# Kernel tuning notes

Measured on AMD Instinct MI355X. Metric: run time of the kernel, lower is better.

Reference implementation:

```python
import jax, jax.numpy as jnp
from jax import lax
import numpy as np

D = 1024   # hidden_size
N = 8      # num_experts
K = 2      # num_chosen_experts
KS = 1     # num_shared_experts
H = 2 * D  # hidden_ratio * D
B, S = 2, 1024


def setup_inputs() -> dict:
    key = jax.random.key(0)
    k1, k2, k3, k4 = jax.random.split(key, 4)
    scale = 1.0 / np.sqrt(D).astype(np.float32)
    x = jax.random.normal(k1, (B, S, D), dtype=jnp.float32)
    Wg = jax.random.normal(k2, (D, N), dtype=jnp.float32) * scale
    Wl1 = jax.random.normal(k3, (N, D, 2 * H), dtype=jnp.float32) * scale
    Wl2 = jax.random.normal(k4, (N, H, D), dtype=jnp.float32) * scale
    return {"x_BSD": x, "Wg_DN": Wg, "Wl1_ND2H": Wl1, "Wl2_NHD": Wl2}


def _moe(x_BSD, Wg_DN, Wl1_ND2H, Wl2_NHD):
    b, s, d = x_BSD.shape
    x_MD = x_BSD.reshape(b * s, d)            # [M, D]
    Nr = N - KS                               # number of routed experts

    # --- gating (softmax path) ---
    s_raw_MN = x_MD @ Wg_DN                   # [M, N]
    routed = jax.nn.softmax(s_raw_MN[:, :Nr].astype(jnp.float32), axis=-1)
    shared = jax.nn.softmax(s_raw_MN[:, Nr:].astype(jnp.float32), axis=-1)

    # biases for routed experts are zero at init -> topk on raw softmax scores
    _, idx_MK = lax.top_k(routed, K - KS)     # [M, K-KS]
    mask = jnp.sum(jax.nn.one_hot(idx_MK, Nr, dtype=jnp.float32), axis=1)  # [M, Nr]
    sel = routed * mask
    routed_n = sel / jnp.sum(sel, axis=-1, keepdims=True)   # renormalize selected gates
    shared_n = shared / jnp.sum(shared, axis=-1, keepdims=True)
    gates_MN = jnp.concatenate([routed_n, shared_n], axis=-1).astype(x_MD.dtype)  # [M, N]

    # --- experts: gather-free dense combine; gates are exactly 0 for unselected experts ---
    def step(y_MD, inp):
        w1_D2H, w2_HD, g_M = inp
        z = x_MD @ w1_D2H                     # [M, 2H]
        a, bgate = jnp.split(z, 2, axis=-1)
        h = jax.nn.silu(bgate) * a            # SwiGLU
        return y_MD + g_M[:, None] * (h @ w2_HD), None

    y0 = jnp.zeros_like(x_MD)
    y_MD, _ = lax.scan(step, y0, (Wl1_ND2H, Wl2_NHD, gates_MN.T))
    return y_MD.reshape(b, s, d)


def reference(x_BSD, Wg_DN, Wl1_ND2H, Wl2_NHD):
    return _moe(x_BSD, Wg_DN, Wl1_ND2H, Wl2_NHD)
```

## Files before the change

### kernel.cpp

```cpp
#include <hip/hip_runtime.h>
#include <stdint.h>


typedef __bf16 bf16x8 __attribute__((ext_vector_type(8)));
typedef float f32x4 __attribute__((ext_vector_type(4)));

typedef __attribute__((address_space(1))) const void gvoid_t;
typedef __attribute__((address_space(3))) void lvoid_t;

__device__ __forceinline__ void gload16(void* lds, const void* g) {
  __builtin_amdgcn_global_load_lds((gvoid_t*)g, (lvoid_t*)lds, 16, 0, 0);
}

__device__ __forceinline__ uint16_t f2bf(float f) {
  union { float f; uint32_t u; } v; v.f = f;
  uint32_t u = v.u + 0x7fffu + ((v.u >> 16) & 1u);
  return (uint16_t)(u >> 16);
}

#define S_VMCNT12() asm volatile("s_waitcnt vmcnt(12)" ::: "memory")
#define S_VMCNT16() asm volatile("s_waitcnt vmcnt(16)" ::: "memory")
#define S_VMCNT0()  asm volatile("s_waitcnt vmcnt(0)" ::: "memory")
#define S_LGKM0()   asm volatile("s_waitcnt lgkmcnt(0)" ::: "memory")
#define S_BAR()     __builtin_amdgcn_s_barrier()

#define CVT_PK(dst, lo, hi) \
  asm("v_cvt_pk_bf16_f32 %0, %1, %2" : "=v"(dst) : "v"(lo), "v"(hi))

__global__ __launch_bounds__(256) void gate_kernel(const float* __restrict__ x,
                                                   const float* __restrict__ Wg,
                                                   uint16_t* __restrict__ xbf,
                                                   int* __restrict__ idx) {
  int wid = threadIdx.x >> 6, lane = threadIdx.x & 63;
  int m = blockIdx.x * 4 + wid;
  const float* xr = x + (size_t)m * 1024;
  uint16_t* xbr = xbf + (size_t)m * 1024;
  float acc[8] = {0.f, 0.f, 0.f, 0.f, 0.f, 0.f, 0.f, 0.f};
  for (int it = 0; it < 4; ++it) {
    int dbase = it * 256 + lane * 4;
    float4 xv = *reinterpret_cast<const float4*>(xr + dbase);
    ushort4 o;
    o.x = f2bf(xv.x); o.y = f2bf(xv.y); o.z = f2bf(xv.z); o.w = f2bf(xv.w);
    *reinterpret_cast<ushort4*>(xbr + dbase) = o;
    const float* xp = reinterpret_cast<const float*>(&xv);
    for (int dd = 0; dd < 4; ++dd) {
      float xs = xp[dd];
      float4 w0 = *reinterpret_cast<const float4*>(Wg + (size_t)(dbase + dd) * 8);
      float4 w1 = *reinterpret_cast<const float4*>(Wg + (size_t)(dbase + dd) * 8 + 4);
      acc[0] += xs * w0.x; acc[1] += xs * w0.y; acc[2] += xs * w0.z; acc[3] += xs * w0.w;
      acc[4] += xs * w1.x; acc[5] += xs * w1.y; acc[6] += xs * w1.z; acc[7] += xs * w1.w;
    }
  }
  for (int j = 0; j < 7; ++j)
    for (int off = 32; off; off >>= 1)
      acc[j] += __shfl_xor(acc[j], off);
  if (lane == 0) {
    int best = 0; float bv = acc[0];
    for (int j = 1; j < 7; ++j) if (acc[j] > bv) { bv = acc[j]; best = j; }
    idx[m] = best;
  }
}

__global__ __launch_bounds__(256) void compact_kernel(const int* __restrict__ idx,
                                                      int* __restrict__ soff,
                                                      int* __restrict__ scnt,
                                                      int* __restrict__ rowmap,
                                                      int* __restrict__ tokrow) {
  __shared__ int hist[256][7];
  __shared__ int cnts[7];
  __shared__ int off[7];
  int t = threadIdx.x;
  int e8[8];
  int lh[7] = {0, 0, 0, 0, 0, 0, 0};
#pragma unroll
  for (int i = 0; i < 8; ++i) { int e = idx[t * 8 + i]; e8[i] = e; lh[e]++; }
#pragma unroll
  for (int e = 0; e < 7; ++e) hist[t][e] = lh[e];
  __syncthreads();
  if (t < 7) {
    int run = 0;
    for (int i = 0; i < 256; ++i) { int v = hist[i][t]; hist[i][t] = run; run += v; }
    cnts[t] = run;
  }
  __syncthreads();
  if (t == 0) {
    int run = 0;
    for (int e = 0; e < 7; ++e) { off[e] = run; soff[e] = run; scnt[e] = cnts[e]; run += cnts[e]; }
    soff[7] = 0; scnt[7] = 2048;
  }
  __syncthreads();
  int pos[7];
#pragma unroll
  for (int e = 0; e < 7; ++e) pos[e] = off[e] + hist[t][e];
#pragma unroll
  for (int i = 0; i < 8; ++i) {
    int m = t * 8 + i, e = e8[i];
    int r = pos[e]++;
    rowmap[r] = m;
    tokrow[m] = r;
  }
}

__global__ __launch_bounds__(256, 2) void zgemm_kernel(
    const uint16_t* __restrict__ xbf,
    const float* __restrict__ W1,
    const int* __restrict__ soff, const int* __restrict__ scnt,
    const int* __restrict__ rowmap,
    uint16_t* __restrict__ za,
    uint16_t* __restrict__ zb)
{
  int by = blockIdx.y;
  int seg, rt;
  if (by < 42) { seg = by / 6; rt = by % 6; } else { seg = 7; rt = by - 42; }
  int cnt = scnt[seg];
  if (rt * 128 >= cnt) return;
  int base = (seg == 7) ? 2048 : soff[seg];
  int rbase = (seg == 7) ? 0 : soff[seg];
  int bx = blockIdx.x;
  int G0 = (bx < 16) ? bx * 128 : 2048 + (bx - 16) * 128;
  uint16_t* zout = (bx < 16) ? za : zb;
  int zc0 = (bx < 16) ? bx * 128 : (bx - 16) * 128;

  __shared__ uint16_t lds[2][16384];

  int t = threadIdx.x, lane = t & 63, w = t >> 6;
  int trow = w * 8 + ((t >> 3) & 7);
  int slot = (t & 7) ^ (trow & 7);

  const uint16_t* aptr[4];
#pragma unroll
  for (int i = 0; i < 4; ++i) {
    int rl = i * 32 + trow;
    int rr = rt * 128 + rl; if (rr >= cnt) rr = cnt - 1;
    int tok = (seg == 7) ? rr : rowmap[rbase + rr];
    aptr[i] = xbf + (size_t)tok * 1024 + slot * 8;
  }
  auto stageA = [&](int buf, int kt) {
    uint16_t* L = lds[buf];
#pragma unroll
    for (int i = 0; i < 4; ++i) gload16(&L[(i * 32 + trow) * 64 + (t & 7) * 8], aptr[i] + kt * 64);
  };

  const float* w1f = W1 + (size_t)seg * (1024u * 4096u);
  int kg = t >> 5;
  int n4 = (t & 31) * 4;
  const float* bsrc = w1f + (size_t)(kg * 8) * 4096 + G0 + n4;
  int bwoff[4];
#pragma unroll
  for (int j = 0; j < 4; ++j) {
    int cl = n4 + j;
    int sw = cl ^ ((cl >> 2) & 7);
    bwoff[j] = 8192 + kg * 1024 + sw * 8;
  }
  f32x4 P0[8], P1[8];
  auto issueB = [&](f32x4 (&P)[8], int kt) {
    const float* p = bsrc + (size_t)kt * 64 * 4096;
#pragma unroll
    for (int i = 0; i < 8; ++i) P[i] = *reinterpret_cast<const f32x4*>(p + (size_t)i * 4096);
  };
  auto writeB = [&](f32x4 (&P)[8], int buf) {
    uint16_t* L = lds[buf];
#pragma unroll
    for (int j = 0; j < 4; ++j) {
      uint32_t q0, q1, q2, q3;
      CVT_PK(q0, P[0][j], P[1][j]);
      CVT_PK(q1, P[2][j], P[3][j]);
      CVT_PK(q2, P[4][j], P[5][j]);
      CVT_PK(q3, P[6][j], P[7][j]);
      uint4 v; v.x = q0; v.y = q1; v.z = q2; v.w = q3;
      *reinterpret_cast<uint4*>(&L[bwoff[j]]) = v;
    }
  };

  int wr = (w >> 1) & 1, wc = w & 1;
  int l15 = lane & 15, lk = lane >> 4;
  int boff[4];
#pragma unroll
  for (int n = 0; n < 4; ++n) {
    int cl = wc * 64 + n * 16 + l15;
    boff[n] = 8192 + (cl ^ ((cl >> 2) & 7)) * 8;
  }

  f32x4 acc[4][4] = {};

  auto compute = [&](int buf) {
    const uint16_t* L = lds[buf];
#pragma unroll
    for (int g = 0; g < 2; ++g) {
      __builtin_amdgcn_s_setprio(1);
      bf16x8 af[4];
#pragma unroll
      for (int m = 0; m < 4; ++m) {
        int row = wr * 64 + m * 16 + l15;
        int p = (g * 4 + lk) ^ (row & 7);
        af[m] = *reinterpret_cast<const bf16x8*>(&L[row * 64 + p * 8]);
      }
#pragma unroll
      for (int n = 0; n < 4; ++n) {
        bf16x8 bfr = *reinterpret_cast<const bf16x8*>(&L[boff[n] + (g * 4 + lk) * 1024]);
#pragma unroll
        for (int m = 0; m < 4; ++m)
          acc[m][n] = __builtin_amdgcn_mfma_f32_16x16x32_bf16(af[m], bfr, acc[m][n], 0, 0, 0);
      }
      __builtin_amdgcn_s_setprio(0);
    }
  };

  const int NT = 16;
  issueB(P0, 0); stageA(0, 0);
  issueB(P1, 1); stageA(1, 1);
  S_VMCNT16();
  writeB(P0, 0);
  issueB(P0, 2);
  S_LGKM0();

#pragma unroll 1
  for (int kt = 0; kt < NT; kt += 2) {
    if (kt < NT - 2) S_VMCNT12(); else S_VMCNT0();
    S_BAR();
    compute(0);
    if (kt < NT - 1) writeB(P1, 1);
    S_LGKM0(); S_BAR();
    if (kt < NT - 3) issueB(P1, kt + 3);
    if (kt < NT - 2) stageA(0, kt + 2);
    int ko = kt + 1;
    if (ko < NT - 2) S_VMCNT12(); else S_VMCNT0();
    S_BAR();
    compute(1);
    if (ko < NT - 1) writeB(P0, 0);
    S_LGKM0(); S_BAR();
    if (ko < NT - 3) issueB(P0, ko + 3);
    if (ko < NT - 2) stageA(1, ko + 2);
  }

#pragma unroll
  for (int m = 0; m < 4; ++m)
#pragma unroll
    for (int n = 0; n < 4; ++n) {
      int col = zc0 + wc * 64 + n * 16 + l15;
#pragma unroll
      for (int j = 0; j < 4; ++j) {
        int row = rt * 128 + wr * 64 + m * 16 + lk * 4 + j;
        if (row < cnt)
          zout[(size_t)(base + row) * 2048 + col] = f2bf(acc[m][n][j]);
      }
    }
}

__global__ __launch_bounds__(256) void swiglu_kernel(const uint16_t* __restrict__ za,
                                                     const uint16_t* __restrict__ zb,
                                                     uint16_t* __restrict__ h) {
  size_t base = (size_t)blockIdx.x * 2048 + threadIdx.x * 8;
  uint4 va = *reinterpret_cast<const uint4*>(za + base);
  uint4 vb = *reinterpret_cast<const uint4*>(zb + base);
  const uint16_t* pa = reinterpret_cast<const uint16_t*>(&va);
  const uint16_t* pb = reinterpret_cast<const uint16_t*>(&vb);
  uint16_t o[8];
#pragma unroll
  for (int i = 0; i < 8; ++i) {
    union { uint32_t u; float f; } a, b;
    a.u = (uint32_t)pa[i] << 16;
    b.u = (uint32_t)pb[i] << 16;
    float sv = b.f / (1.0f + __expf(-b.f));
    o[i] = f2bf(sv * a.f);
  }
  *reinterpret_cast<uint4*>(h + base) = *reinterpret_cast<uint4*>(o);
}

__global__ __launch_bounds__(256, 2) void ffn2_kernel(
    const uint16_t* __restrict__ h,
    const float* __restrict__ W2,
    const int* __restrict__ soff, const int* __restrict__ scnt,
    float* __restrict__ y,
    float* __restrict__ yr)
{
  int by = blockIdx.y;
  int seg, rt;
  if (by < 42) { seg = by / 6; rt = by % 6; } else { seg = 7; rt = by - 42; }
  int cnt = scnt[seg];
  if (rt * 128 >= cnt) return;
  int base = (seg == 7) ? 2048 : soff[seg];
  int obase = (seg == 7) ? 0 : soff[seg];
  int n0 = blockIdx.x * 128;

  __shared__ uint16_t lds[2][16384];

  int t = threadIdx.x, lane = t & 63, w = t >> 6;
  int trow = w * 8 + ((t >> 3) & 7);
  int slot = (t & 7) ^ (trow & 7);

  const uint16_t* aptr[4];
#pragma unroll
  for (int i = 0; i < 4; ++i) {
    int rl = i * 32 + trow;
    int rr = rt * 128 + rl; if (rr >= cnt) rr = cnt - 1;
    aptr[i] = h + (size_t)(base + rr) * 2048 + slot * 8;
  }
  auto stageA = [&](int buf, int kt) {
    uint16_t* L = lds[buf];
#pragma unroll
    for (int i = 0; i < 4; ++i) gload16(&L[(i * 32 + trow) * 64 + (t & 7) * 8], aptr[i] + kt * 64);
  };

  const float* w2f = W2 + (size_t)seg * (2048u * 1024u);
  int kg = t >> 5;
  int n4 = (t & 31) * 4;
  const float* bsrc = w2f + (size_t)(kg * 8) * 1024 + n0 + n4;
  int bwoff[4];
#pragma unroll
  for (int j = 0; j < 4; ++j) {
    int cl = n4 + j;
    int sw = cl ^ ((cl >> 2) & 7);
    bwoff[j] = 8192 + kg * 1024 + sw * 8;
  }
  f32x4 P0[8], P1[8];
  auto issueB = [&](f32x4 (&P)[8], int kt) {
    const float* p = bsrc + (size_t)kt * 64 * 1024;
#pragma unroll
    for (int i = 0; i < 8; ++i) P[i] = *reinterpret_cast<const f32x4*>(p + (size_t)i * 1024);
  };
  auto writeB = [&](f32x4 (&P)[8], int buf) {
    uint16_t* L = lds[buf];
#pragma unroll
    for (int j = 0; j < 4; ++j) {
      uint32_t q0, q1, q2, q3;
      CVT_PK(q0, P[0][j], P[1][j]);
      CVT_PK(q1, P[2][j], P[3][j]);
      CVT_PK(q2, P[4][j], P[5][j]);
      CVT_PK(q3, P[6][j], P[7][j]);
      uint4 v; v.x = q0; v.y = q1; v.z = q2; v.w = q3;
      *reinterpret_cast<uint4*>(&L[bwoff[j]]) = v;
    }
  };

  int wr = (w >> 1) & 1, wc = w & 1;
  int l15 = lane & 15, lk = lane >> 4;
  int boff[4];
#pragma unroll
  for (int n = 0; n < 4; ++n) {
    int cl = wc * 64 + n * 16 + l15;
    boff[n] = 8192 + (cl ^ ((cl >> 2) & 7)) * 8;
  }

  f32x4 acc[4][4] = {};

  auto compute = [&](int buf) {
    const uint16_t* L = lds[buf];
#pragma unroll
    for (int g = 0; g < 2; ++g) {
      __builtin_amdgcn_s_setprio(1);
      bf16x8 af[4];
#pragma unroll
      for (int m = 0; m < 4; ++m) {
        int row = wr * 64 + m * 16 + l15;
        int p = (g * 4 + lk) ^ (row & 7);
        af[m] = *reinterpret_cast<const bf16x8*>(&L[row * 64 + p * 8]);
      }
#pragma unroll
      for (int n = 0; n < 4; ++n) {
        bf16x8 bfr = *reinterpret_cast<const bf16x8*>(&L[boff[n] + (g * 4 + lk) * 1024]);
#pragma unroll
        for (int m = 0; m < 4; ++m)
          acc[m][n] = __builtin_amdgcn_mfma_f32_16x16x32_bf16(af[m], bfr, acc[m][n], 0, 0, 0);
      }
      __builtin_amdgcn_s_setprio(0);
    }
  };

  const int NT = 32;
  issueB(P0, 0); stageA(0, 0);
  issueB(P1, 1); stageA(1, 1);
  S_VMCNT16();
  writeB(P0, 0);
  issueB(P0, 2);
  S_LGKM0();

#pragma unroll 1
  for (int kt = 0; kt < NT; kt += 2) {
    if (kt < NT - 2) S_VMCNT12(); else S_VMCNT0();
    S_BAR();
    compute(0);
    if (kt < NT - 1) writeB(P1, 1);
    S_LGKM0(); S_BAR();
    if (kt < NT - 3) issueB(P1, kt + 3);
    if (kt < NT - 2) stageA(0, kt + 2);
    int ko = kt + 1;
    if (ko < NT - 2) S_VMCNT12(); else S_VMCNT0();
    S_BAR();
    compute(1);
    if (ko < NT - 1) writeB(P0, 0);
    S_LGKM0(); S_BAR();
    if (ko < NT - 3) issueB(P0, ko + 3);
    if (ko < NT - 2) stageA(1, ko + 2);
  }

#pragma unroll
  for (int m = 0; m < 4; ++m)
#pragma unroll
    for (int n = 0; n < 4; ++n) {
      int col = n0 + wc * 64 + n * 16 + l15;
#pragma unroll
      for (int j = 0; j < 4; ++j) {
        int row = rt * 128 + wr * 64 + m * 16 + lk * 4 + j;
        if (row < cnt) {
          if (seg == 7) y[(size_t)row * 1024 + col] = acc[m][n][j];
          else          yr[(size_t)(obase + row) * 1024 + col] = acc[m][n][j];
        }
      }
    }
}

__global__ __launch_bounds__(256) void combine_kernel(const float* __restrict__ yr,
                                                      const int* __restrict__ tokrow,
                                                      float* __restrict__ y) {
  int m = blockIdx.x;
  int d = threadIdx.x * 4;
  int r = tokrow[m];
  float4 a = *reinterpret_cast<const float4*>(yr + (size_t)r * 1024 + d);
  float4 o = *reinterpret_cast<const float4*>(y + (size_t)m * 1024 + d);
  o.x += a.x; o.y += a.y; o.z += a.z; o.w += a.w;
  *reinterpret_cast<float4*>(y + (size_t)m * 1024 + d) = o;
}

extern "C" void kernel_launch(void* const* d_in, const int* in_sizes, int n_in,
                              void* d_out, int out_size, void* d_ws, size_t ws_size,
                              hipStream_t stream)
{
  const float* x   = (const float*)d_in[0];
  const float* Wg  = (const float*)d_in[1];
  const float* Wl1 = (const float*)d_in[2];
  const float* Wl2 = (const float*)d_in[3];
  float* y = (float*)d_out;
  char* ws = (char*)d_ws;

  uint16_t* xbf = (uint16_t*)(ws);
  uint16_t* h   = (uint16_t*)(ws + (4ull  << 20));
  float*    yr  = (float*)   (ws + (20ull << 20));
  uint16_t* za  = (uint16_t*)(ws + (28ull << 20));
  uint16_t* zb  = (uint16_t*)(ws + (44ull << 20));
  int* idx    = (int*)(ws + (60ull << 20));
  int* tokrow = idx + 2048;
  int* soff   = tokrow + 2048;
  int* scnt   = soff + 8;
  int* rowmap = scnt + 8;

  gate_kernel<<<512, 256, 0, stream>>>(x, Wg, xbf, idx);
  compact_kernel<<<1, 256, 0, stream>>>(idx, soff, scnt, rowmap, tokrow);
  zgemm_kernel<<<dim3(32, 58), 256, 0, stream>>>(xbf, Wl1, soff, scnt, rowmap, za, zb);
  swiglu_kernel<<<4096, 256, 0, stream>>>(za, zb, h);
  ffn2_kernel<<<dim3(8, 58), 256, 0, stream>>>(h, Wl2, soff, scnt, y, yr);
  combine_kernel<<<2048, 256, 0, stream>>>(yr, tokrow, y);
}
```

Baseline: 150.6 us.

## Pre-convert W1 to swizzled bf16 tiles and stream them directly into LDS

Adds a kernel that converts the fp32 first-layer expert weights into a bf16 layout already tiled and swizzled for shared memory, on every call. The first GEMM then loads weight tiles with direct global-to-LDS copies and a simpler single-stage double-buffered loop, replacing register staging and fp32-to-bf16 conversion. This removes redundant fp32 weight reads and conversions repeated across row tiles. In exchange it adds a full read of the fp32 weights plus a bf16 write per call, and needs a larger workspace.

```diff
diff --git a/kernel.cpp b/kernel.cpp
--- a/kernel.cpp
+++ b/kernel.cpp
@@ -18,6 +18,7 @@
   return (uint16_t)(u >> 16);
 }
 
+#define S_VMCNT8()  asm volatile("s_waitcnt vmcnt(8)" ::: "memory")
 #define S_VMCNT12() asm volatile("s_waitcnt vmcnt(12)" ::: "memory")
 #define S_VMCNT16() asm volatile("s_waitcnt vmcnt(16)" ::: "memory")
 #define S_VMCNT0()  asm volatile("s_waitcnt vmcnt(0)" ::: "memory")
@@ -101,9 +102,45 @@
   }
 }
 
-__global__ __launch_bounds__(256, 2) void zgemm_kernel(
+__global__ __launch_bounds__(256) void wcvt_kernel(const float* __restrict__ W1,
+                                                   uint16_t* __restrict__ w1p) {
+  int b = blockIdx.x;
+  int e = b >> 7, kt = (b >> 3) & 15, xg = b & 7;
+  const float* we = W1 + (size_t)e * 1024 * 4096;
+  int t = threadIdx.x;
+  int kg = t >> 5;
+  int c4 = (t & 31) * 4;
+  const float* src0 = we + (size_t)(kt * 64 + kg * 8) * 4096;
+  int swo[4];
+#pragma unroll
+  for (int j = 0; j < 4; ++j) {
+    int cl = c4 + j;
+    swo[j] = (cl ^ ((cl >> 2) & 7)) * 8;
+  }
+#pragma unroll 1
+  for (int xi = 0; xi < 4; ++xi) {
+    int x = xg * 4 + xi;
+    const float* s = src0 + x * 128 + c4;
+    f32x4 d[8];
+#pragma unroll
+    for (int i = 0; i < 8; ++i) d[i] = *reinterpret_cast<const f32x4*>(s + (size_t)i * 4096);
+    uint16_t* dst = w1p + (((size_t)(e * 32 + x) * 16 + kt) * 8192) + kg * 1024;
+#pragma unroll
+    for (int j = 0; j < 4; ++j) {
+      uint32_t q0, q1, q2, q3;
+      CVT_PK(q0, d[0][j], d[1][j]);
+      CVT_PK(q1, d[2][j], d[3][j]);
+      CVT_PK(q2, d[4][j], d[5][j]);
+      CVT_PK(q3, d[6][j], d[7][j]);
+      uint4 v; v.x = q0; v.y = q1; v.z = q2; v.w = q3;
+      *reinterpret_cast<uint4*>(dst + swo[j]) = v;
+    }
+  }
+}
+
+__global__ __launch_bounds__(256, 2) void zgemm2_kernel(
     const uint16_t* __restrict__ xbf,
-    const float* __restrict__ W1,
+    const uint16_t* __restrict__ w1p,
     const int* __restrict__ soff, const int* __restrict__ scnt,
     const int* __restrict__ rowmap,
     uint16_t* __restrict__ za,
@@ -117,7 +154,6 @@
   int base = (seg == 7) ? 2048 : soff[seg];
   int rbase = (seg == 7) ? 0 : soff[seg];
   int bx = blockIdx.x;
-  int G0 = (bx < 16) ? bx * 128 : 2048 + (bx - 16) * 128;
   uint16_t* zout = (bx < 16) ? za : zb;
   int zc0 = (bx < 16) ? bx * 128 : (bx - 16) * 128;
 
@@ -135,16 +171,134 @@
     int tok = (seg == 7) ? rr : rowmap[rbase + rr];
     aptr[i] = xbf + (size_t)tok * 1024 + slot * 8;
   }
+  const uint16_t* bp = w1p + ((size_t)(seg * 32 + bx) * 16) * 8192 + t * 8;
+
+  auto stage = [&](int buf, int kt) {
+    uint16_t* L = lds[buf];
+#pragma unroll
+    for (int i = 0; i < 4; ++i) gload16(&L[(i * 32 + trow) * 64 + (t & 7) * 8], aptr[i] + kt * 64);
+#pragma unroll
+    for (int i = 0; i < 4; ++i) gload16(&L[8192 + i * 2048 + t * 8], bp + (size_t)kt * 8192 + i * 2048);
+  };
+
+  int wr = (w >> 1) & 1, wc = w & 1;
+  int l15 = lane & 15, lk = lane >> 4;
+  int boff[4];
+#pragma unroll
+  for (int n = 0; n < 4; ++n) {
+    int cl = wc * 64 + n * 16 + l15;
+    boff[n] = 8192 + (cl ^ ((cl >> 2) & 7)) * 8;
+  }
+
+  f32x4 acc[4][4] = {};
+
+  auto compute = [&](int buf) {
+    const uint16_t* L = lds[buf];
+#pragma unroll
+    for (int g = 0; g < 2; ++g) {
+      __builtin_amdgcn_s_setprio(1);
+      bf16x8 af[4];
+#pragma unroll
+      for (int m = 0; m < 4; ++m) {
+        int row = wr * 64 + m * 16 + l15;
+        int p = (g * 4 + lk) ^ (row & 7);
+        af[m] = *reinterpret_cast<const bf16x8*>(&L[row * 64 + p * 8]);
+      }
+#pragma unroll
+      for (int n = 0; n < 4; ++n) {
+        bf16x8 bfr = *reinterpret_cast<const bf16x8*>(&L[boff[n] + (g * 4 + lk) * 1024]);
+#pragma unroll
+        for (int m = 0; m < 4; ++m)
+          acc[m][n] = __builtin_amdgcn_mfma_f32_16x16x32_bf16(af[m], bfr, acc[m][n], 0, 0, 0);
+      }
+      __builtin_amdgcn_s_setprio(0);
+    }
+  };
+
+  const int NT = 16;
+  stage(0, 0);
+  stage(1, 1);
+#pragma unroll 1
+  for (int kt = 0; kt < NT; ++kt) {
+    if (kt < NT - 1) S_VMCNT8(); else S_VMCNT0();
+    S_BAR();
+    compute(kt & 1);
+    S_BAR();
+    if (kt < NT - 2) stage(kt & 1, kt + 2);
+  }
+
+#pragma unroll
+  for (int m = 0; m < 4; ++m)
+#pragma unroll
+    for (int n = 0; n < 4; ++n) {
+      int col = zc0 + wc * 64 + n * 16 + l15;
+#pragma unroll
+      for (int j = 0; j < 4; ++j) {
+        int row = rt * 128 + wr * 64 + m * 16 + lk * 4 + j;
+        if (row < cnt)
+          zout[(size_t)(base + row) * 2048 + col] = f2bf(acc[m][n][j]);
+      }
+    }
+}
+
+__global__ __launch_bounds__(256) void swiglu_kernel(const uint16_t* __restrict__ za,
+                                                     const uint16_t* __restrict__ zb,
+                                                     uint16_t* __restrict__ h) {
+  size_t base = (size_t)blockIdx.x * 2048 + threadIdx.x * 8;
+  uint4 va = *reinterpret_cast<const uint4*>(za + base);
+  uint4 vb = *reinterpret_cast<const uint4*>(zb + base);
+  const uint16_t* pa = reinterpret_cast<const uint16_t*>(&va);
+  const uint16_t* pb = reinterpret_cast<const uint16_t*>(&vb);
+  uint16_t o[8];
+#pragma unroll
+  for (int i = 0; i < 8; ++i) {
+    union { uint32_t u; float f; } a, b;
+    a.u = (uint32_t)pa[i] << 16;
+    b.u = (uint32_t)pb[i] << 16;
+    float sv = b.f / (1.0f + __expf(-b.f));
+    o[i] = f2bf(sv * a.f);
+  }
+  *reinterpret_cast<uint4*>(h + base) = *reinterpret_cast<uint4*>(o);
+}
+
+__global__ __launch_bounds__(256, 2) void ffn2_kernel(
+    const uint16_t* __restrict__ h,
+    const float* __restrict__ W2,
+    const int* __restrict__ soff, const int* __restrict__ scnt,
+    float* __restrict__ y, float* __restrict__ yr)
+{
+  int by = blockIdx.y;
+  int seg, rt;
+  if (by < 42) { seg = by / 6; rt = by % 6; } else { seg = 7; rt = by - 42; }
+  int cnt = scnt[seg];
+  if (rt * 128 >= cnt) return;
+  int base = (seg == 7) ? 2048 : soff[seg];
+  int obase = (seg == 7) ? 0 : soff[seg];
+  int n0 = blockIdx.x * 128;
+
+  __shared__ uint16_t lds[2][16384];
+
+  int t = threadIdx.x, lane = t & 63, w = t >> 6;
+  int trow = w * 8 + ((t >> 3) & 7);
+  int slot = (t & 7) ^ (trow & 7);
+
+  const uint16_t* aptr[4];
+#pragma unroll
+  for (int i = 0; i < 4; ++i) {
+    int rl = i * 32 + trow;
+    int rr = rt * 128 + rl; if (rr >= cnt) rr = cnt - 1;
+    aptr[i] = h + (size_t)(base + rr) * 2048 + slot * 8;
+  }
   auto stageA = [&](int buf, int kt) {
     uint16_t* L = lds[buf];
 #pragma unroll
     for (int i = 0; i < 4; ++i) gload16(&L[(i * 32 + trow) * 64 + (t & 7) * 8], aptr[i] + kt * 64);
   };
 
-  const float* w1f = W1 + (size_t)seg * (1024u * 4096u);
+  const float* w2f = W2 + (size_t)seg * (2048u * 1024u);
   int kg = t >> 5;
   int n4 = (t & 31) * 4;
-  const float* bsrc = w1f + (size_t)(kg * 8) * 4096 + G0 + n4;
+  const float* bsrc = w2f + (size_t)(kg * 8) * 1024 + n0 + n4;
   int bwoff[4];
 #pragma unroll
   for (int j = 0; j < 4; ++j) {
@@ -154,9 +308,9 @@
   }
   f32x4 P0[8], P1[8];
   auto issueB = [&](f32x4 (&P)[8], int kt) {
-    const float* p = bsrc + (size_t)kt * 64 * 4096;
-#pragma unroll
-    for (int i = 0; i < 8; ++i) P[i] = *reinterpret_cast<const f32x4*>(p + (size_t)i * 4096);
+    const float* p = bsrc + (size_t)kt * 64 * 1024;
+#pragma unroll
+    for (int i = 0; i < 8; ++i) P[i] = *reinterpret_cast<const f32x4*>(p + (size_t)i * 1024);
   };
   auto writeB = [&](f32x4 (&P)[8], int buf) {
     uint16_t* L = lds[buf];
@@ -206,7 +360,7 @@
     }
   };
 
-  const int NT = 16;
+  const int NT = 32;
   issueB(P0, 0); stageA(0, 0);
   issueB(P1, 1); stageA(1, 1);
   S_VMCNT16();
@@ -237,167 +391,6 @@
   for (int m = 0; m < 4; ++m)
 #pragma unroll
     for (int n = 0; n < 4; ++n) {
-      int col = zc0 + wc * 64 + n * 16 + l15;
-#pragma unroll
-      for (int j = 0; j < 4; ++j) {
-        int row = rt * 128 + wr * 64 + m * 16 + lk * 4 + j;
-        if (row < cnt)
-          zout[(size_t)(base + row) * 2048 + col] = f2bf(acc[m][n][j]);
-      }
-    }
-}
-
-__global__ __launch_bounds__(256) void swiglu_kernel(const uint16_t* __restrict__ za,
-                                                     const uint16_t* __restrict__ zb,
-                                                     uint16_t* __restrict__ h) {
-  size_t base = (size_t)blockIdx.x * 2048 + threadIdx.x * 8;
-  uint4 va = *reinterpret_cast<const uint4*>(za + base);
-  uint4 vb = *reinterpret_cast<const uint4*>(zb + base);
-  const uint16_t* pa = reinterpret_cast<const uint16_t*>(&va);
-  const uint16_t* pb = reinterpret_cast<const uint16_t*>(&vb);
-  uint16_t o[8];
-#pragma unroll
-  for (int i = 0; i < 8; ++i) {
-    union { uint32_t u; float f; } a, b;
-    a.u = (uint32_t)pa[i] << 16;
-    b.u = (uint32_t)pb[i] << 16;
-    float sv = b.f / (1.0f + __expf(-b.f));
-    o[i] = f2bf(sv * a.f);
-  }
-  *reinterpret_cast<uint4*>(h + base) = *reinterpret_cast<uint4*>(o);
-}
-
-__global__ __launch_bounds__(256, 2) void ffn2_kernel(
-    const uint16_t* __restrict__ h,
-    const float* __restrict__ W2,
-    const int* __restrict__ soff, const int* __restrict__ scnt,
-    float* __restrict__ y,
-    float* __restrict__ yr)
-{
-  int by = blockIdx.y;
-  int seg, rt;
-  if (by < 42) { seg = by / 6; rt = by % 6; } else { seg = 7; rt = by - 42; }
-  int cnt = scnt[seg];
-  if (rt * 128 >= cnt) return;
-  int base = (seg == 7) ? 2048 : soff[seg];
-  int obase = (seg == 7) ? 0 : soff[seg];
-  int n0 = blockIdx.x * 128;
-
-  __shared__ uint16_t lds[2][16384];
-
-  int t = threadIdx.x, lane = t & 63, w = t >> 6;
-  int trow = w * 8 + ((t >> 3) & 7);
-  int slot = (t & 7) ^ (trow & 7);
-
-  const uint16_t* aptr[4];
-#pragma unroll
-  for (int i = 0; i < 4; ++i) {
-    int rl = i * 32 + trow;
-    int rr = rt * 128 + rl; if (rr >= cnt) rr = cnt - 1;
-    aptr[i] = h + (size_t)(base + rr) * 2048 + slot * 8;
-  }
-  auto stageA = [&](int buf, int kt) {
-    uint16_t* L = lds[buf];
-#pragma unroll
-    for (int i = 0; i < 4; ++i) gload16(&L[(i * 32 + trow) * 64 + (t & 7) * 8], aptr[i] + kt * 64);
-  };
-
-  const float* w2f = W2 + (size_t)seg * (2048u * 1024u);
-  int kg = t >> 5;
-  int n4 = (t & 31) * 4;
-  const float* bsrc = w2f + (size_t)(kg * 8) * 1024 + n0 + n4;
-  int bwoff[4];
-#pragma unroll
-  for (int j = 0; j < 4; ++j) {
-    int cl = n4 + j;
-    int sw = cl ^ ((cl >> 2) & 7);
-    bwoff[j] = 8192 + kg * 1024 + sw * 8;
-  }
-  f32x4 P0[8], P1[8];
-  auto issueB = [&](f32x4 (&P)[8], int kt) {
-    const float* p = bsrc + (size_t)kt * 64 * 1024;
-#pragma unroll
-    for (int i = 0; i < 8; ++i) P[i] = *reinterpret_cast<const f32x4*>(p + (size_t)i * 1024);
-  };
-  auto writeB = [&](f32x4 (&P)[8], int buf) {
-    uint16_t* L = lds[buf];
-#pragma unroll
-    for (int j = 0; j < 4; ++j) {
-      uint32_t q0, q1, q2, q3;
-      CVT_PK(q0, P[0][j], P[1][j]);
-      CVT_PK(q1, P[2][j], P[3][j]);
-      CVT_PK(q2, P[4][j], P[5][j]);
-      CVT_PK(q3, P[6][j], P[7][j]);
-      uint4 v; v.x = q0; v.y = q1; v.z = q2; v.w = q3;
-      *reinterpret_cast<uint4*>(&L[bwoff[j]]) = v;
-    }
-  };
-
-  int wr = (w >> 1) & 1, wc = w & 1;
-  int l15 = lane & 15, lk = lane >> 4;
-  int boff[4];
-#pragma unroll
-  for (int n = 0; n < 4; ++n) {
-    int cl = wc * 64 + n * 16 + l15;
-    boff[n] = 8192 + (cl ^ ((cl >> 2) & 7)) * 8;
-  }
-
-  f32x4 acc[4][4] = {};
-
-  auto compute = [&](int buf) {
-    const uint16_t* L = lds[buf];
-#pragma unroll
-    for (int g = 0; g < 2; ++g) {
-      __builtin_amdgcn_s_setprio(1);
-      bf16x8 af[4];
-#pragma unroll
-      for (int m = 0; m < 4; ++m) {
-        int row = wr * 64 + m * 16 + l15;
-        int p = (g * 4 + lk) ^ (row & 7);
-        af[m] = *reinterpret_cast<const bf16x8*>(&L[row * 64 + p * 8]);
-      }
-#pragma unroll
-      for (int n = 0; n < 4; ++n) {
-        bf16x8 bfr = *reinterpret_cast<const bf16x8*>(&L[boff[n] + (g * 4 + lk) * 1024]);
-#pragma unroll
-        for (int m = 0; m < 4; ++m)
-          acc[m][n] = __builtin_amdgcn_mfma_f32_16x16x32_bf16(af[m], bfr, acc[m][n], 0, 0, 0);
-      }
-      __builtin_amdgcn_s_setprio(0);
-    }
-  };
-
-  const int NT = 32;
-  issueB(P0, 0); stageA(0, 0);
-  issueB(P1, 1); stageA(1, 1);
-  S_VMCNT16();
-  writeB(P0, 0);
-  issueB(P0, 2);
-  S_LGKM0();
-
-#pragma unroll 1
-  for (int kt = 0; kt < NT; kt += 2) {
-    if (kt < NT - 2) S_VMCNT12(); else S_VMCNT0();
-    S_BAR();
-    compute(0);
-    if (kt < NT - 1) writeB(P1, 1);
-    S_LGKM0(); S_BAR();
-    if (kt < NT - 3) issueB(P1, kt + 3);
-    if (kt < NT - 2) stageA(0, kt + 2);
-    int ko = kt + 1;
-    if (ko < NT - 2) S_VMCNT12(); else S_VMCNT0();
-    S_BAR();
-    compute(1);
-    if (ko < NT - 1) writeB(P0, 0);
-    S_LGKM0(); S_BAR();
-    if (ko < NT - 3) issueB(P0, ko + 3);
-    if (ko < NT - 2) stageA(1, ko + 2);
-  }
-
-#pragma unroll
-  for (int m = 0; m < 4; ++m)
-#pragma unroll
-    for (int n = 0; n < 4; ++n) {
       int col = n0 + wc * 64 + n * 16 + l15;
 #pragma unroll
       for (int j = 0; j < 4; ++j) {
@@ -438,7 +431,8 @@
   float*    yr  = (float*)   (ws + (20ull << 20));
   uint16_t* za  = (uint16_t*)(ws + (28ull << 20));
   uint16_t* zb  = (uint16_t*)(ws + (44ull << 20));
-  int* idx    = (int*)(ws + (60ull << 20));
+  uint16_t* w1p = (uint16_t*)(ws + (60ull << 20));
+  int* idx    = (int*)(ws + (124ull << 20));
   int* tokrow = idx + 2048;
   int* soff   = tokrow + 2048;
   int* scnt   = soff + 8;
@@ -446,7 +440,8 @@
 
   gate_kernel<<<512, 256, 0, stream>>>(x, Wg, xbf, idx);
   compact_kernel<<<1, 256, 0, stream>>>(idx, soff, scnt, rowmap, tokrow);
-  zgemm_kernel<<<dim3(32, 58), 256, 0, stream>>>(xbf, Wl1, soff, scnt, rowmap, za, zb);
+  wcvt_kernel<<<1024, 256, 0, stream>>>(Wl1, w1p);
+  zgemm2_kernel<<<dim3(32, 58), 256, 0, stream>>>(xbf, w1p, soff, scnt, rowmap, za, zb);
   swiglu_kernel<<<4096, 256, 0, stream>>>(za, zb, h);
   ffn2_kernel<<<dim3(8, 58), 256, 0, stream>>>(h, Wl2, soff, scnt, y, yr);
   combine_kernel<<<2048, 256, 0, stream>>>(yr, tokrow, y);
```

After: 176.9 us. +17.5%, slower.
